# Performance work log

Hardware: AMD Instinct MI355X
Metric: run time of the kernel (lower is better)

Reference implementation:

```python
import jax, jax.numpy as jnp
import numpy as np

Z_RES, N_RES = 128, 512
M_PTS = 2_000_000


def trilinear_devoxelize(grid, coords):
    """Gather-based trilinear interpolation.
    grid:   (Z, N, N, C) voxel grid
    coords: (M, 3) float positions in voxel index space (z, x, y)
    returns (M, C)
    """
    Zd, Nd = grid.shape[0], grid.shape[1]
    c0f = jnp.floor(coords)
    frac = coords - c0f                      # (M, 3) fractional offsets
    maxi = jnp.array([Zd - 1, Nd - 1, Nd - 1], dtype=jnp.int32)
    c0 = jnp.clip(c0f.astype(jnp.int32), 0, maxi)
    c1 = jnp.clip(c0 + 1, 0, maxi)
    fz, fx, fy = frac[:, 0:1], frac[:, 1:2], frac[:, 2:3]
    gz, gx, gy = 1.0 - fz, 1.0 - fx, 1.0 - fy

    def g(zi, xi, yi):
        return grid[zi, xi, yi]              # (M, C) gather

    out = (g(c0[:, 0], c0[:, 1], c0[:, 2]) * gz * gx * gy
         + g(c0[:, 0], c0[:, 1], c1[:, 2]) * gz * gx * fy
         + g(c0[:, 0], c1[:, 1], c0[:, 2]) * gz * fx * gy
         + g(c0[:, 0], c1[:, 1], c1[:, 2]) * gz * fx * fy
         + g(c1[:, 0], c0[:, 1], c0[:, 2]) * fz * gx * gy
         + g(c1[:, 0], c0[:, 1], c1[:, 2]) * fz * gx * fy
         + g(c1[:, 0], c1[:, 1], c0[:, 2]) * fz * fx * gy
         + g(c1[:, 0], c1[:, 1], c1[:, 2]) * fz * fx * fy)
    return out


def setup_inputs() -> dict:
    key = jax.random.key(0)
    k1, k2 = jax.random.split(key)
    extents = jnp.array([Z_RES - 1, N_RES - 1, N_RES - 1], jnp.float32)
    coords = jax.random.uniform(k1, (M_PTS, 3), dtype=jnp.float32) * extents
    # init_scale = 1.0 -> albedo ~ U[0,1); normal initialized to zeros (per module)
    albedo = jax.random.uniform(k2, (Z_RES, N_RES, N_RES), dtype=jnp.float32)
    normal = jnp.zeros((Z_RES, N_RES, N_RES, 3), dtype=jnp.float32)
    return {"coords": coords, "albedo": albedo, "normal": normal}


def reference(coords, albedo, normal):
    base_normal = jnp.array([-1.0, 0.0, 0.0], dtype=jnp.float32)
    a = trilinear_devoxelize(albedo[..., None], coords)[:, 0]   # (M,)
    n = trilinear_devoxelize(normal, coords)                    # (M, 3)
    a = jax.nn.elu(a)
    n = jnp.tanh(n) + base_normal
    # F.normalize(dim=1, eps=1e-12): divide by max(||n||, eps)
    norm = jnp.maximum(jnp.linalg.norm(n, axis=1, keepdims=True), 1e-12)
    n = n / norm
    return (a, n)
```

## Files before the change

kernel.cpp:

```cpp
#include <hip/hip_runtime.h>
#include <math.h>

#define ZR 128
#define NR 512

__global__ __launch_bounds__(256) void zcheck_kernel(
    const uint4* __restrict__ normal4, unsigned int* __restrict__ flag, long long n4)
{
    long long stride = (long long)gridDim.x * 256;
    unsigned int acc = 0;
    for (long long i = (long long)blockIdx.x * 256 + threadIdx.x; i < n4; i += stride) {
        uint4 v = normal4[i];
        acc |= v.x | v.y | v.z | v.w;
    }
    unsigned long long any = __ballot(acc != 0);
    if (any && ((threadIdx.x & 63) == 0)) {
        atomicOr(flag, 1u);
    }
}

__global__ __launch_bounds__(256) void interp_fast_kernel(
    const float* __restrict__ coords,
    const float* __restrict__ albedo,
    const unsigned int* __restrict__ flag,
    float* __restrict__ out_a,
    float* __restrict__ out_n,
    int M)
{
    if (*flag != 0) return;

    int i = blockIdx.x * 256 + threadIdx.x;
    if (i >= M) return;

    float cz = coords[3 * i + 0];
    float cx = coords[3 * i + 1];
    float cy = coords[3 * i + 2];

    float fz0 = floorf(cz), fx0 = floorf(cx), fy0 = floorf(cy);
    float fz = cz - fz0, fx = cx - fx0, fy = cy - fy0;

    int z0 = min(max((int)fz0, 0), ZR - 1);
    int x0 = min(max((int)fx0, 0), NR - 1);
    int y0 = min(max((int)fy0, 0), NR - 1);
    int z1 = min(z0 + 1, ZR - 1);
    int x1 = min(x0 + 1, NR - 1);
    int y1 = min(y0 + 1, NR - 1);

    float gz = 1.0f - fz, gx = 1.0f - fx, gy = 1.0f - fy;

    float w000 = gz * gx * gy, w001 = gz * gx * fy;
    float w010 = gz * fx * gy, w011 = gz * fx * fy;
    float w100 = fz * gx * gy, w101 = fz * gx * fy;
    float w110 = fz * fx * gy, w111 = fz * fx * fy;

    size_t b00 = ((size_t)z0 * NR + x0) * NR;
    size_t b01 = ((size_t)z0 * NR + x1) * NR;
    size_t b10 = ((size_t)z1 * NR + x0) * NR;
    size_t b11 = ((size_t)z1 * NR + x1) * NR;

    float a =
        albedo[b00 + y0] * w000 + albedo[b00 + y1] * w001 +
        albedo[b01 + y0] * w010 + albedo[b01 + y1] * w011 +
        albedo[b10 + y0] * w100 + albedo[b10 + y1] * w101 +
        albedo[b11 + y0] * w110 + albedo[b11 + y1] * w111;

    a = (a > 0.0f) ? a : expm1f(a);

    out_a[i] = a;
    out_n[3 * i + 0] = -1.0f;
    out_n[3 * i + 1] = 0.0f;
    out_n[3 * i + 2] = 0.0f;
}

__global__ __launch_bounds__(256) void interp_full_kernel(
    const float* __restrict__ coords,
    const float* __restrict__ albedo,
    const float* __restrict__ normal,
    const unsigned int* __restrict__ flag,
    float* __restrict__ out_a,
    float* __restrict__ out_n,
    int M)
{
    if (*flag == 0) return;

    int i = blockIdx.x * 256 + threadIdx.x;
    if (i >= M) return;

    float cz = coords[3 * i + 0];
    float cx = coords[3 * i + 1];
    float cy = coords[3 * i + 2];

    float fz0 = floorf(cz), fx0 = floorf(cx), fy0 = floorf(cy);
    float fz = cz - fz0, fx = cx - fx0, fy = cy - fy0;

    int z0 = min(max((int)fz0, 0), ZR - 1);
    int x0 = min(max((int)fx0, 0), NR - 1);
    int y0 = min(max((int)fy0, 0), NR - 1);
    int z1 = min(z0 + 1, ZR - 1);
    int x1 = min(x0 + 1, NR - 1);
    int y1 = min(y0 + 1, NR - 1);

    float gz = 1.0f - fz, gx = 1.0f - fx, gy = 1.0f - fy;

    float w000 = gz * gx * gy, w001 = gz * gx * fy;
    float w010 = gz * fx * gy, w011 = gz * fx * fy;
    float w100 = fz * gx * gy, w101 = fz * gx * fy;
    float w110 = fz * fx * gy, w111 = fz * fx * fy;

    size_t b00 = ((size_t)z0 * NR + x0) * NR;
    size_t b01 = ((size_t)z0 * NR + x1) * NR;
    size_t b10 = ((size_t)z1 * NR + x0) * NR;
    size_t b11 = ((size_t)z1 * NR + x1) * NR;

    float a =
        albedo[b00 + y0] * w000 + albedo[b00 + y1] * w001 +
        albedo[b01 + y0] * w010 + albedo[b01 + y1] * w011 +
        albedo[b10 + y0] * w100 + albedo[b10 + y1] * w101 +
        albedo[b11 + y0] * w110 + albedo[b11 + y1] * w111;

    float n0 = 0.0f, n1 = 0.0f, n2 = 0.0f;
#define ACC(base, yy, w)                                        \
    {                                                           \
        const float* q = normal + ((base) + (size_t)(yy)) * 3;  \
        n0 += q[0] * (w);                                       \
        n1 += q[1] * (w);                                       \
        n2 += q[2] * (w);                                       \
    }
    ACC(b00, y0, w000); ACC(b00, y1, w001);
    ACC(b01, y0, w010); ACC(b01, y1, w011);
    ACC(b10, y0, w100); ACC(b10, y1, w101);
    ACC(b11, y0, w110); ACC(b11, y1, w111);
#undef ACC

    a = (a > 0.0f) ? a : expm1f(a);

    n0 = tanhf(n0) - 1.0f;
    n1 = tanhf(n1);
    n2 = tanhf(n2);

    float nrm = sqrtf(n0 * n0 + n1 * n1 + n2 * n2);
    nrm = fmaxf(nrm, 1e-12f);
    float inv = 1.0f / nrm;

    out_a[i] = a;
    out_n[3 * i + 0] = n0 * inv;
    out_n[3 * i + 1] = n1 * inv;
    out_n[3 * i + 2] = n2 * inv;
}

extern "C" void kernel_launch(void* const* d_in, const int* in_sizes, int n_in,
                              void* d_out, int out_size, void* d_ws, size_t ws_size,
                              hipStream_t stream) {
    const float* coords = (const float*)d_in[0];
    const float* albedo = (const float*)d_in[1];
    const float* normal = (const float*)d_in[2];

    int M = in_sizes[0] / 3;
    long long normal_elems = (long long)in_sizes[2];
    long long n4 = normal_elems / 4;

    float* out = (float*)d_out;
    float* out_a = out;
    float* out_n = out + M;

    unsigned int* flag = (unsigned int*)d_ws;
    hipMemsetAsync(flag, 0, sizeof(unsigned int), stream);

    zcheck_kernel<<<4096, 256, 0, stream>>>((const uint4*)normal, flag, n4);

    int nblk = (M + 255) / 256;
    interp_fast_kernel<<<nblk, 256, 0, stream>>>(coords, albedo, flag, out_a, out_n, M);
    interp_full_kernel<<<nblk, 256, 0, stream>>>(coords, albedo, normal, flag, out_a, out_n, M);
}
```

Baseline: 746.5 us.

## Fuse zero-check scan with albedo interpolation in one persistent kernel

Merges the normal-grid zero scan and the albedo interpolation into one persistent kernel. One quarter of the blocks scan the normal grid with nontemporal vector loads while the other three quarters run the albedo gather, so the streaming read and the random gather overlap instead of running one after the other. A separate grid-stride kernel writes the normal output only when the flag is set, and it overwrites the default normals. This removes one launch and the serial dependency on the scan. The cost is a fixed block split that may not balance the two workloads.

```diff
diff --git a/kernel.cpp b/kernel.cpp
--- a/kernel.cpp
+++ b/kernel.cpp
@@ -3,149 +3,146 @@
 
 #define ZR 128
 #define NR 512
+#define NBLK 4096
 
-__global__ __launch_bounds__(256) void zcheck_kernel(
-    const uint4* __restrict__ normal4, unsigned int* __restrict__ flag, long long n4)
+typedef unsigned int u32x4 __attribute__((ext_vector_type(4)));
+
+__global__ __launch_bounds__(256) void fused_kernel(
+    const float* __restrict__ coords,
+    const float* __restrict__ albedo,
+    const u32x4* __restrict__ normal4,
+    const unsigned int* __restrict__ normal_tail,
+    int tail_cnt,
+    unsigned int* __restrict__ flag,
+    float* __restrict__ out_a,
+    float* __restrict__ out_n,
+    int M, long long n4)
 {
-    long long stride = (long long)gridDim.x * 256;
-    unsigned int acc = 0;
-    for (long long i = (long long)blockIdx.x * 256 + threadIdx.x; i < n4; i += stride) {
-        uint4 v = normal4[i];
-        acc |= v.x | v.y | v.z | v.w;
+    unsigned int b = blockIdx.x;
+    if ((b & 3u) == 1u) {
+        long long zrank = b >> 2;
+        long long nthreads = (long long)(NBLK / 4) * 256;
+        unsigned int acc = 0;
+        for (long long i = zrank * 256 + threadIdx.x; i < n4; i += nthreads) {
+            u32x4 v = __builtin_nontemporal_load(&normal4[i]);
+            acc |= v.x | v.y | v.z | v.w;
+        }
+        if (zrank == 0 && threadIdx.x < (unsigned)tail_cnt)
+            acc |= normal_tail[threadIdx.x];
+        if (__ballot(acc != 0) && ((threadIdx.x & 63) == 0))
+            atomicOr(flag, 1u);
+        return;
     }
-    unsigned long long any = __ballot(acc != 0);
-    if (any && ((threadIdx.x & 63) == 0)) {
-        atomicOr(flag, 1u);
+    unsigned int g = b >> 2;
+    unsigned int sub = b & 3u;
+    unsigned int irank = g * 3u + (sub == 0u ? 0u : sub - 1u);
+    int stride = (NBLK / 4 * 3) * 256;
+
+    for (int i = (int)(irank * 256u + threadIdx.x); i < M; i += stride) {
+        float cz = coords[3 * i + 0];
+        float cx = coords[3 * i + 1];
+        float cy = coords[3 * i + 2];
+
+        float fz0 = floorf(cz), fx0 = floorf(cx), fy0 = floorf(cy);
+        float fz = cz - fz0, fx = cx - fx0, fy = cy - fy0;
+
+        int z0 = min(max((int)fz0, 0), ZR - 1);
+        int x0 = min(max((int)fx0, 0), NR - 1);
+        int y0 = min(max((int)fy0, 0), NR - 1);
+        int z1 = min(z0 + 1, ZR - 1);
+        int x1 = min(x0 + 1, NR - 1);
+        int y1 = min(y0 + 1, NR - 1);
+
+        float gz = 1.0f - fz, gx = 1.0f - fx, gy = 1.0f - fy;
+
+        float w000 = gz * gx * gy, w001 = gz * gx * fy;
+        float w010 = gz * fx * gy, w011 = gz * fx * fy;
+        float w100 = fz * gx * gy, w101 = fz * gx * fy;
+        float w110 = fz * fx * gy, w111 = fz * fx * fy;
+
+        size_t b00 = ((size_t)z0 * NR + x0) * NR;
+        size_t b01 = ((size_t)z0 * NR + x1) * NR;
+        size_t b10 = ((size_t)z1 * NR + x0) * NR;
+        size_t b11 = ((size_t)z1 * NR + x1) * NR;
+
+        float a =
+            albedo[b00 + y0] * w000 + albedo[b00 + y1] * w001 +
+            albedo[b01 + y0] * w010 + albedo[b01 + y1] * w011 +
+            albedo[b10 + y0] * w100 + albedo[b10 + y1] * w101 +
+            albedo[b11 + y0] * w110 + albedo[b11 + y1] * w111;
+
+        a = (a > 0.0f) ? a : expm1f(a);
+
+        out_a[i] = a;
+        out_n[3 * i + 0] = -1.0f;
+        out_n[3 * i + 1] = 0.0f;
+        out_n[3 * i + 2] = 0.0f;
     }
 }
 
-__global__ __launch_bounds__(256) void interp_fast_kernel(
+__global__ __launch_bounds__(256) void normal_full_kernel(
     const float* __restrict__ coords,
-    const float* __restrict__ albedo,
-    const unsigned int* __restrict__ flag,
-    float* __restrict__ out_a,
-    float* __restrict__ out_n,
-    int M)
-{
-    if (*flag != 0) return;
-
-    int i = blockIdx.x * 256 + threadIdx.x;
-    if (i >= M) return;
-
-    float cz = coords[3 * i + 0];
-    float cx = coords[3 * i + 1];
-    float cy = coords[3 * i + 2];
-
-    float fz0 = floorf(cz), fx0 = floorf(cx), fy0 = floorf(cy);
-    float fz = cz - fz0, fx = cx - fx0, fy = cy - fy0;
-
-    int z0 = min(max((int)fz0, 0), ZR - 1);
-    int x0 = min(max((int)fx0, 0), NR - 1);
-    int y0 = min(max((int)fy0, 0), NR - 1);
-    int z1 = min(z0 + 1, ZR - 1);
-    int x1 = min(x0 + 1, NR - 1);
-    int y1 = min(y0 + 1, NR - 1);
-
-    float gz = 1.0f - fz, gx = 1.0f - fx, gy = 1.0f - fy;
-
-    float w000 = gz * gx * gy, w001 = gz * gx * fy;
-    float w010 = gz * fx * gy, w011 = gz * fx * fy;
-    float w100 = fz * gx * gy, w101 = fz * gx * fy;
-    float w110 = fz * fx * gy, w111 = fz * fx * fy;
-
-    size_t b00 = ((size_t)z0 * NR + x0) * NR;
-    size_t b01 = ((size_t)z0 * NR + x1) * NR;
-    size_t b10 = ((size_t)z1 * NR + x0) * NR;
-    size_t b11 = ((size_t)z1 * NR + x1) * NR;
-
-    float a =
-        albedo[b00 + y0] * w000 + albedo[b00 + y1] * w001 +
-        albedo[b01 + y0] * w010 + albedo[b01 + y1] * w011 +
-        albedo[b10 + y0] * w100 + albedo[b10 + y1] * w101 +
-        albedo[b11 + y0] * w110 + albedo[b11 + y1] * w111;
-
-    a = (a > 0.0f) ? a : expm1f(a);
-
-    out_a[i] = a;
-    out_n[3 * i + 0] = -1.0f;
-    out_n[3 * i + 1] = 0.0f;
-    out_n[3 * i + 2] = 0.0f;
-}
-
-__global__ __launch_bounds__(256) void interp_full_kernel(
-    const float* __restrict__ coords,
-    const float* __restrict__ albedo,
     const float* __restrict__ normal,
     const unsigned int* __restrict__ flag,
-    float* __restrict__ out_a,
     float* __restrict__ out_n,
     int M)
 {
     if (*flag == 0) return;
 
-    int i = blockIdx.x * 256 + threadIdx.x;
-    if (i >= M) return;
+    int stride = gridDim.x * 256;
+    for (int i = blockIdx.x * 256 + threadIdx.x; i < M; i += stride) {
+        float cz = coords[3 * i + 0];
+        float cx = coords[3 * i + 1];
+        float cy = coords[3 * i + 2];
 
-    float cz = coords[3 * i + 0];
-    float cx = coords[3 * i + 1];
-    float cy = coords[3 * i + 2];
+        float fz0 = floorf(cz), fx0 = floorf(cx), fy0 = floorf(cy);
+        float fz = cz - fz0, fx = cx - fx0, fy = cy - fy0;
 
-    float fz0 = floorf(cz), fx0 = floorf(cx), fy0 = floorf(cy);
-    float fz = cz - fz0, fx = cx - fx0, fy = cy - fy0;
+        int z0 = min(max((int)fz0, 0), ZR - 1);
+        int x0 = min(max((int)fx0, 0), NR - 1);
+        int y0 = min(max((int)fy0, 0), NR - 1);
+        int z1 = min(z0 + 1, ZR - 1);
+        int x1 = min(x0 + 1, NR - 1);
+        int y1 = min(y0 + 1, NR - 1);
 
-    int z0 = min(max((int)fz0, 0), ZR - 1);
-    int x0 = min(max((int)fx0, 0), NR - 1);
-    int y0 = min(max((int)fy0, 0), NR - 1);
-    int z1 = min(z0 + 1, ZR - 1);
-    int x1 = min(x0 + 1, NR - 1);
-    int y1 = min(y0 + 1, NR - 1);
+        float gz = 1.0f - fz, gx = 1.0f - fx, gy = 1.0f - fy;
 
-    float gz = 1.0f - fz, gx = 1.0f - fx, gy = 1.0f - fy;
+        float w000 = gz * gx * gy, w001 = gz * gx * fy;
+        float w010 = gz * fx * gy, w011 = gz * fx * fy;
+        float w100 = fz * gx * gy, w101 = fz * gx * fy;
+        float w110 = fz * fx * gy, w111 = fz * fx * fy;
 
-    float w000 = gz * gx * gy, w001 = gz * gx * fy;
-    float w010 = gz * fx * gy, w011 = gz * fx * fy;
-    float w100 = fz * gx * gy, w101 = fz * gx * fy;
-    float w110 = fz * fx * gy, w111 = fz * fx * fy;
+        size_t b00 = ((size_t)z0 * NR + x0) * NR;
+        size_t b01 = ((size_t)z0 * NR + x1) * NR;
+        size_t b10 = ((size_t)z1 * NR + x0) * NR;
+        size_t b11 = ((size_t)z1 * NR + x1) * NR;
 
-    size_t b00 = ((size_t)z0 * NR + x0) * NR;
-    size_t b01 = ((size_t)z0 * NR + x1) * NR;
-    size_t b10 = ((size_t)z1 * NR + x0) * NR;
-    size_t b11 = ((size_t)z1 * NR + x1) * NR;
-
-    float a =
-        albedo[b00 + y0] * w000 + albedo[b00 + y1] * w001 +
-        albedo[b01 + y0] * w010 + albedo[b01 + y1] * w011 +
-        albedo[b10 + y0] * w100 + albedo[b10 + y1] * w101 +
-        albedo[b11 + y0] * w110 + albedo[b11 + y1] * w111;
-
-    float n0 = 0.0f, n1 = 0.0f, n2 = 0.0f;
+        float n0 = 0.0f, n1 = 0.0f, n2 = 0.0f;
 #define ACC(base, yy, w)                                        \
-    {                                                           \
-        const float* q = normal + ((base) + (size_t)(yy)) * 3;  \
-        n0 += q[0] * (w);                                       \
-        n1 += q[1] * (w);                                       \
-        n2 += q[2] * (w);                                       \
-    }
-    ACC(b00, y0, w000); ACC(b00, y1, w001);
-    ACC(b01, y0, w010); ACC(b01, y1, w011);
-    ACC(b10, y0, w100); ACC(b10, y1, w101);
-    ACC(b11, y0, w110); ACC(b11, y1, w111);
+        {                                                       \
+            const float* q = normal + ((base) + (size_t)(yy)) * 3; \
+            n0 += q[0] * (w);                                   \
+            n1 += q[1] * (w);                                   \
+            n2 += q[2] * (w);                                   \
+        }
+        ACC(b00, y0, w000); ACC(b00, y1, w001);
+        ACC(b01, y0, w010); ACC(b01, y1, w011);
+        ACC(b10, y0, w100); ACC(b10, y1, w101);
+        ACC(b11, y0, w110); ACC(b11, y1, w111);
 #undef ACC
 
-    a = (a > 0.0f) ? a : expm1f(a);
+        n0 = tanhf(n0) - 1.0f;
+        n1 = tanhf(n1);
+        n2 = tanhf(n2);
 
-    n0 = tanhf(n0) - 1.0f;
-    n1 = tanhf(n1);
-    n2 = tanhf(n2);
+        float nrm = sqrtf(n0 * n0 + n1 * n1 + n2 * n2);
+        nrm = fmaxf(nrm, 1e-12f);
+        float inv = 1.0f / nrm;
 
-    float nrm = sqrtf(n0 * n0 + n1 * n1 + n2 * n2);
-    nrm = fmaxf(nrm, 1e-12f);
-    float inv = 1.0f / nrm;
-
-    out_a[i] = a;
-    out_n[3 * i + 0] = n0 * inv;
-    out_n[3 * i + 1] = n1 * inv;
-    out_n[3 * i + 2] = n2 * inv;
+        out_n[3 * i + 0] = n0 * inv;
+        out_n[3 * i + 1] = n1 * inv;
+        out_n[3 * i + 2] = n2 * inv;
+    }
 }
 
 extern "C" void kernel_launch(void* const* d_in, const int* in_sizes, int n_in,
@@ -158,6 +155,8 @@
     int M = in_sizes[0] / 3;
     long long normal_elems = (long long)in_sizes[2];
     long long n4 = normal_elems / 4;
+    int tail_cnt = (int)(normal_elems & 3);
+    const unsigned int* normal_tail = (const unsigned int*)normal + n4 * 4;
 
     float* out = (float*)d_out;
     float* out_a = out;
@@ -166,9 +165,9 @@
     unsigned int* flag = (unsigned int*)d_ws;
     hipMemsetAsync(flag, 0, sizeof(unsigned int), stream);
 
-    zcheck_kernel<<<4096, 256, 0, stream>>>((const uint4*)normal, flag, n4);
+    fused_kernel<<<NBLK, 256, 0, stream>>>(
+        coords, albedo, (const u32x4*)normal, normal_tail, tail_cnt,
+        flag, out_a, out_n, M, n4);
 
-    int nblk = (M + 255) / 256;
-    interp_fast_kernel<<<nblk, 256, 0, stream>>>(coords, albedo, flag, out_a, out_n, M);
-    interp_full_kernel<<<nblk, 256, 0, stream>>>(coords, albedo, normal, flag, out_a, out_n, M);
+    normal_full_kernel<<<2048, 256, 0, stream>>>(coords, normal, flag, out_n, M);
 }
```

Measured after the change: 702.8 us. 5.9% less time.
